# Performance work log

Hardware: AMD Instinct MI355X
Metric: run time of the kernel (lower is better)

## Reference

```python
import jax, jax.numpy as jnp
import numpy as np

N_NODES = 6144
IN_FEATURES = 256
N_HEADS = 4
N_HIDDEN = 64  # out_features, concat=False
LEAKY_SLOPE = 0.2
NEG_INF = -9e16


def setup_inputs() -> dict:
    key = jax.random.key(0)
    k1, k2, k3, k4 = jax.random.split(key, 4)
    h = jax.random.normal(k1, (N_NODES, IN_FEATURES), dtype=jnp.float32)
    adj_mat = jax.random.randint(k2, (N_NODES, N_NODES), 0, 2, dtype=jnp.int32)
    W = jax.random.normal(k3, (IN_FEATURES, N_HEADS * N_HIDDEN), dtype=jnp.float32) * 0.06
    a = jax.random.normal(k4, (N_HEADS, 2 * N_HIDDEN, 1), dtype=jnp.float32) * 0.1
    return {"h": h, "adj_mat": adj_mat, "W": W, "a": a}


def reference(h, adj_mat, W, a):
    n_nodes = h.shape[0]
    # linear transform, dropout is identity in eval mode
    ht = (h @ W).reshape(n_nodes, N_HEADS, N_HIDDEN).transpose(1, 0, 2)  # [H, N, d]
    a_src = a[:, :N_HIDDEN, 0]   # [H, d]
    a_tgt = a[:, N_HIDDEN:, 0]   # [H, d]
    src = jnp.einsum('hnd,hd->hn', ht, a_src)  # [H, N]
    tgt = jnp.einsum('hnd,hd->hn', ht, a_tgt)  # [H, N]
    e = src[:, :, None] + tgt[:, None, :]       # [H, N, N]
    e = jnp.where(e >= 0, e, LEAKY_SLOPE * e)    # leaky relu
    e = jnp.where(adj_mat[None, :, :] > 0, e, jnp.float32(NEG_INF))
    attention = jax.nn.softmax(e, axis=-1)       # [H, N, N]
    h_prime = jnp.einsum('hij,hjd->hid', attention, ht)  # [H, N, d]
    return h_prime.mean(axis=0)                  # [N, d] (concat=False)
```

## Files before the change

kernel.cpp:

```cpp
#include <hip/hip_runtime.h>
#include <hip/hip_bf16.h>

#define N_NODES 6144
#define IN_F 256
#define N_HEADS 4
#define N_HID 64
#define JS 8
#define JLEN (N_NODES / JS)
#define NW (JLEN / 32)
#define SM_STRIDE 28

typedef __attribute__((ext_vector_type(4))) float floatx4;
typedef _Float16 half2_t __attribute__((ext_vector_type(2)));
typedef _Float16 half8_t __attribute__((ext_vector_type(8)));
typedef __attribute__((ext_vector_type(4))) unsigned uint4_t;
typedef short short2v __attribute__((ext_vector_type(2)));

__global__ __launch_bounds__(256) void ht_gemm_kernel(
    const float* __restrict__ h, const float* __restrict__ W,
    const float* __restrict__ a, short* __restrict__ htF,
    float* __restrict__ srcv, unsigned* __restrict__ tE1pk, unsigned* __restrict__ tE2pk)
{
    __shared__ float As[32][34];
    __shared__ float Bs[32][68];
    __shared__ float redS[32][16];
    __shared__ float redT[32][16];
    __shared__ unsigned short eh1[32], eh2[32];

    const int head = blockIdx.y;
    const int i0 = blockIdx.x * 32;
    const int tid = threadIdx.x;
    const int tx = tid & 15, ty = tid >> 4;

    float acc[2][4] = {};

    for (int k0 = 0; k0 < IN_F; k0 += 32) {
        __syncthreads();
        {
            const int m = tid >> 3, kq = tid & 7;
            const float4 v = *(const float4*)(h + (i0 + m) * IN_F + k0 + kq * 4);
            As[kq*4+0][m] = v.x; As[kq*4+1][m] = v.y;
            As[kq*4+2][m] = v.z; As[kq*4+3][m] = v.w;
        }
        #pragma unroll
        for (int it = 0; it < 2; ++it) {
            int l = it * 256 + tid;
            int k = l >> 4, nq = l & 15;
            *(float4*)&Bs[k][nq*4] = *(const float4*)(W + (k0 + k) * 256 + head * 64 + nq * 4);
        }
        __syncthreads();
        #pragma unroll
        for (int kk = 0; kk < 32; ++kk) {
            const float2 av = *(const float2*)&As[kk][ty*2];
            const float4 bv = *(const float4*)&Bs[kk][tx*4];
            const float aa[2] = {av.x, av.y};
            const float bb[4] = {bv.x, bv.y, bv.z, bv.w};
            #pragma unroll
            for (int r = 0; r < 2; ++r)
                #pragma unroll
                for (int c = 0; c < 4; ++c)
                    acc[r][c] = fmaf(aa[r], bb[c], acc[r][c]);
        }
    }

    #pragma unroll
    for (int r = 0; r < 2; ++r)
        #pragma unroll
        for (int c2 = 0; c2 < 4; ++c2) {
            const int d = tx * 4 + c2;
            const int j = i0 + ty * 2 + r;
            const int jt = j >> 5, q = (j >> 3) & 3, u = j & 7;
            const int c = d >> 4, n = d & 15;
            const size_t F = (((((size_t)head * 192 + jt) * 4 + c) * 16 + n) * 4 + q) * 8 + u;
            const _Float16 hv = (_Float16)acc[r][c2];
            htF[F] = *(const short*)&hv;
        }

    float as_[4], at_[4];
    #pragma unroll
    for (int c = 0; c < 4; ++c) {
        as_[c] = a[head * 128 + tx * 4 + c];
        at_[c] = a[head * 128 + 64 + tx * 4 + c];
    }
    #pragma unroll
    for (int r = 0; r < 2; ++r) {
        float ps = 0.f, pt = 0.f;
        #pragma unroll
        for (int c = 0; c < 4; ++c) {
            ps = fmaf(acc[r][c], as_[c], ps);
            pt = fmaf(acc[r][c], at_[c], pt);
        }
        redS[ty*2+r][tx] = ps;
        redT[ty*2+r][tx] = pt;
    }
    __syncthreads();
    if (tid < 64) {
        const int row = tid & 31;
        const float* src = (tid < 32) ? &redS[row][0] : &redT[row][0];
        float s = 0.f;
        #pragma unroll
        for (int x = 0; x < 16; ++x) s += src[x];
        if (tid < 32) {
            srcv[head * N_NODES + i0 + row] = s;
        } else {
            const _Float16 E1 = (_Float16)__expf(s);
            const _Float16 E2 = (_Float16)__expf(0.2f * s);
            eh1[row] = *(const unsigned short*)&E1;
            eh2[row] = *(const unsigned short*)&E2;
        }
    }
    __syncthreads();
    if (tid < 16) {
        const unsigned v1 = (unsigned)eh1[2*tid] | ((unsigned)eh1[2*tid+1] << 16);
        const unsigned v2 = (unsigned)eh2[2*tid] | ((unsigned)eh2[2*tid+1] << 16);
        tE1pk[head * (N_NODES/2) + i0/2 + tid] = v1;
        tE2pk[head * (N_NODES/2) + i0/2 + tid] = v2;
    }
}

__global__ __launch_bounds__(256, 3) void gat_main_kernel(
    const int* __restrict__ adj, const short* __restrict__ htF,
    const float* __restrict__ srcv, const unsigned* __restrict__ tE1pk,
    const unsigned* __restrict__ tE2pk,
    float* __restrict__ pnum, float* __restrict__ pden)
{
    __shared__ unsigned smask[64 * SM_STRIDE];
    __shared__ unsigned sE1[4 * 384], sE2[4 * 384];

    const int bid = blockIdx.x;
    const int xcd = bid & 7;
    const int idx = bid >> 3;
    const int jc = idx / 12;
    const int rb0 = ((idx % 12) * 8 + xcd) * 64;

    const int lane = threadIdx.x;
    const int head = threadIdx.y;
    const int m = lane & 15, quad = lane >> 4;
    const int jbase = jc * JLEN;
    const int tid = head * 64 + lane;

    const int* adjb = adj + (size_t)rb0 * N_NODES + jbase + lane;
    for (int k0 = 0; k0 < 192; k0 += 8) {
        int v[8];
        #pragma unroll
        for (int s = 0; s < 8; ++s) {
            const int f = (k0 + s) * 4 + head;
            const int r = f / 12, W = f % 12;
            v[s] = adjb[(size_t)r * N_NODES + W * 64];
        }
        #pragma unroll
        for (int s = 0; s < 8; ++s) {
            const unsigned long long b = __ballot(v[s] > 0);
            const int f = (k0 + s) * 4 + head;
            const int r = f / 12, W = f % 12;
            if (lane == 0)
                *(unsigned long long*)&smask[r * SM_STRIDE + 2 * W] = b;
        }
    }
    #pragma unroll
    for (int it = 0; it < 3; ++it) {
        const int flat = it * 256 + tid;
        const int isE2 = flat >= 384;
        const int f = isE2 ? flat - 384 : flat;
        const int hh = f / 96, w4 = f % 96;
        const unsigned* g = (isE2 ? tE2pk : tE1pk) + hh * (N_NODES/2) + (jbase >> 1) + w4 * 4;
        const uint4_t v = *(const uint4_t*)g;
        unsigned* dst = (isE2 ? sE2 : sE1) + hh * 384 + w4 * 4;
        dst[0] = v.x; dst[1] = v.y; dst[2] = v.z; dst[3] = v.w;
    }
    __syncthreads();

    half2_t e1s[4], e2s[4];
    #pragma unroll
    for (int t = 0; t < 4; ++t) {
        const float sv = srcv[head * N_NODES + rb0 + t * 16 + m];
        const _Float16 a1 = (_Float16)__expf(sv);
        const _Float16 a2 = (_Float16)__expf(0.2f * sv);
        e1s[t] = (half2_t){a1, a1};
        e2s[t] = (half2_t){a2, a2};
    }

    const short* fb = htF + ((size_t)(head * 192 + (jbase >> 5)) * 4) * 512 + (m * 4 + quad) * 8;
    const unsigned* mrow = &smask[m * SM_STRIDE];
    const unsigned* pe1 = &sE1[head * 384];
    const unsigned* pe2 = &sE2[head * 384];

    half8_t bones;
    #pragma unroll
    for (int u = 0; u < 8; ++u) bones[u] = (_Float16)1.0f;

    floatx4 accN[4][4];
    floatx4 accD[4];
    #pragma unroll
    for (int t = 0; t < 4; ++t) {
        accD[t] = (floatx4){0,0,0,0};
        #pragma unroll
        for (int c = 0; c < 4; ++c) accN[t][c] = (floatx4){0,0,0,0};
    }

    half8_t bn[4];
    #pragma unroll
    for (int c = 0; c < 4; ++c) bn[c] = *(const half8_t*)(fb + c * 512);

    for (int w = 0; w < NW; ++w) {
        half8_t bc[4];
        #pragma unroll
        for (int c = 0; c < 4; ++c) bc[c] = bn[c];
        const int wn = (w + 1 < NW) ? (w + 1) : w;
        #pragma unroll
        for (int c = 0; c < 4; ++c)
            bn[c] = *(const half8_t*)(fb + (size_t)wn * 2048 + c * 512);

        const uint4_t E1 = *(const uint4_t*)(pe1 + w * 16 + quad * 4);
        const uint4_t E2 = *(const uint4_t*)(pe2 + w * 16 + quad * 4);
        const unsigned E1a[4] = {E1.x, E1.y, E1.z, E1.w};
        const unsigned E2a[4] = {E2.x, E2.y, E2.z, E2.w};

        #pragma unroll
        for (int t = 0; t < 4; ++t) {
            const unsigned bits = (mrow[t * (16*SM_STRIDE) + w] >> (quad * 8)) & 0xffu;
            const short2v tt = __builtin_bit_cast(short2v, bits * 0x10001u);
            uint4_t af_u;
            #pragma unroll
            for (int p = 0; p < 4; ++p) {
                const short2v shl = (p == 0) ? (short2v){15,14} : (p == 1) ? (short2v){13,12}
                                 : (p == 2) ? (short2v){11,10} : (short2v){9,8};
                const short2v k = (tt << shl) >> (short2v){15,15};
                const half2_t p1 = __builtin_bit_cast(half2_t, E1a[p]) * e1s[t];
                const half2_t p2 = __builtin_bit_cast(half2_t, E2a[p]) * e2s[t];
                const half2_t mx = __builtin_elementwise_max(p1, p2);
                const unsigned r = __builtin_bit_cast(unsigned, mx) & __builtin_bit_cast(unsigned, k);
                if (p == 0) af_u.x = r; else if (p == 1) af_u.y = r;
                else if (p == 2) af_u.z = r; else af_u.w = r;
            }
            const half8_t af = __builtin_bit_cast(half8_t, af_u);
            #pragma unroll
            for (int c = 0; c < 4; ++c)
                accN[t][c] = __builtin_amdgcn_mfma_f32_16x16x32_f16(af, bc[c], accN[t][c], 0, 0, 0);
            accD[t] = __builtin_amdgcn_mfma_f32_16x16x32_f16(af, bones, accD[t], 0, 0, 0);
        }
    }

    const int slot = jc * N_HEADS + head;
    #pragma unroll
    for (int t = 0; t < 4; ++t) {
        if (m == 0) {
            #pragma unroll
            for (int r = 0; r < 4; ++r)
                pden[slot * N_NODES + rb0 + t * 16 + quad * 4 + r] = accD[t][r];
        }
        #pragma unroll
        for (int r = 0; r < 4; ++r) {
            const int gi = rb0 + t * 16 + quad * 4 + r;
            float* np_ = pnum + ((size_t)slot * N_NODES + gi) * N_HID + m;
            np_[0]  = accN[t][0][r];
            np_[16] = accN[t][1][r];
            np_[32] = accN[t][2][r];
            np_[48] = accN[t][3][r];
        }
    }
}

__global__ __launch_bounds__(256) void finalize_kernel(
    const float* __restrict__ pnum, const float* __restrict__ pden,
    float* __restrict__ out)
{
    const int idx = blockIdx.x * 256 + threadIdx.x;
    if (idx >= N_NODES * 16) return;
    const int i = idx >> 4;
    const int d4 = (idx & 15) * 4;
    float sx = 0.f, sy = 0.f, sz = 0.f, sw = 0.f;
    #pragma unroll
    for (int hh = 0; hh < N_HEADS; ++hh) {
        float nx = 0.f, ny = 0.f, nz = 0.f, nw_ = 0.f, ds = 0.f;
        #pragma unroll
        for (int jc = 0; jc < JS; ++jc) {
            const int slot = jc * N_HEADS + hh;
            const float4 v = *(const float4*)(pnum + ((size_t)slot * N_NODES + i) * N_HID + d4);
            nx += v.x; ny += v.y; nz += v.z; nw_ += v.w;
            ds += pden[slot * N_NODES + i];
        }
        const float r = 1.0f / ds;
        sx += nx * r; sy += ny * r; sz += nz * r; sw += nw_ * r;
    }
    float4 o; o.x = 0.25f * sx; o.y = 0.25f * sy; o.z = 0.25f * sz; o.w = 0.25f * sw;
    *(float4*)(out + (size_t)i * N_HID + d4) = o;
}

extern "C" void kernel_launch(void* const* d_in, const int* in_sizes, int n_in,
                              void* d_out, int out_size, void* d_ws, size_t ws_size,
                              hipStream_t stream)
{
    const float* h   = (const float*)d_in[0];
    const int*   adj = (const int*)d_in[1];
    const float* W   = (const float*)d_in[2];
    const float* a   = (const float*)d_in[3];
    float* out = (float*)d_out;

    char* ws = (char*)d_ws;
    short* htF = (short*)ws;
    size_t off = (size_t)N_HEADS * N_HID * N_NODES * 2;
    float* srcv = (float*)(ws + off);        off += (size_t)N_HEADS * N_NODES * 4;
    unsigned* tE1pk = (unsigned*)(ws + off); off += (size_t)N_HEADS * (N_NODES/2) * 4;
    unsigned* tE2pk = (unsigned*)(ws + off); off += (size_t)N_HEADS * (N_NODES/2) * 4;
    float* pnum = (float*)(ws + off);        off += (size_t)JS * N_HEADS * N_NODES * N_HID * 4;
    float* pden = (float*)(ws + off);

    ht_gemm_kernel<<<dim3(N_NODES / 32, N_HEADS), 256, 0, stream>>>(h, W, a, htF, srcv, tE1pk, tE2pk);
    gat_main_kernel<<<768, dim3(64, 4), 0, stream>>>(
        adj, htF, srcv, tE1pk, tE2pk, pnum, pden);
    finalize_kernel<<<dim3((N_NODES * 16 + 255) / 256), 256, 0, stream>>>(pnum, pden, out);
}
```

Before: 270.7 us.

## Pack adjacency mask in prep kernel and reduce split-K partials with atomics

Moves adjacency-to-bitmask packing out of the attention kernel into extra blocks of the GEMM prep kernel, which also zero the accumulators. The main kernel now uses 32-row tiles with higher occupancy, loads the precomputed mask, and prefetches E1/E2 directly from global memory. Split-K partial numerators and denominators are combined with float atomic adds instead of separate per-slice buffers, shrinking the finalize pass. This trades large partial-buffer traffic for atomic contention and nondeterministic summation order.

```diff
diff --git a/kernel.cpp b/kernel.cpp
--- a/kernel.cpp
+++ b/kernel.cpp
@@ -8,7 +8,10 @@
 #define JS 8
 #define JLEN (N_NODES / JS)
 #define NW (JLEN / 32)
-#define SM_STRIDE 28
+#define SM_STRIDE 25
+#define PACK_BLOCKS 768
+#define ACC_F32 (N_HEADS * N_NODES * N_HID + N_HEADS * N_NODES)
+#define ZERO_F4_PER_BLOCK 520
 
 typedef __attribute__((ext_vector_type(4))) float floatx4;
 typedef _Float16 half2_t __attribute__((ext_vector_type(2)));
@@ -16,10 +19,16 @@
 typedef __attribute__((ext_vector_type(4))) unsigned uint4_t;
 typedef short short2v __attribute__((ext_vector_type(2)));
 
-__global__ __launch_bounds__(256) void ht_gemm_kernel(
+__device__ __forceinline__ void atomAddF32(float* p, float v) {
+    unsafeAtomicAdd(p, v);
+}
+
+__global__ __launch_bounds__(256) void prep_kernel(
     const float* __restrict__ h, const float* __restrict__ W,
-    const float* __restrict__ a, short* __restrict__ htF,
-    float* __restrict__ srcv, unsigned* __restrict__ tE1pk, unsigned* __restrict__ tE2pk)
+    const float* __restrict__ a, const int* __restrict__ adj,
+    short* __restrict__ htF, float* __restrict__ srcv,
+    unsigned* __restrict__ tE1pk, unsigned* __restrict__ tE2pk,
+    unsigned long long* __restrict__ gmask, float* __restrict__ accZero)
 {
     __shared__ float As[32][34];
     __shared__ float Bs[32][68];
@@ -27,8 +36,39 @@
     __shared__ float redT[32][16];
     __shared__ unsigned short eh1[32], eh2[32];
 
-    const int head = blockIdx.y;
-    const int i0 = blockIdx.x * 32;
+    if (blockIdx.x < PACK_BLOCKS) {
+        {
+            float4* z = (float4*)accZero + (size_t)blockIdx.x * ZERO_F4_PER_BLOCK;
+            const float4 zv = {0.f, 0.f, 0.f, 0.f};
+            for (int i = threadIdx.x; i < ZERO_F4_PER_BLOCK; i += 256) z[i] = zv;
+        }
+        const int lane = threadIdx.x & 63;
+        const int wave = threadIdx.x >> 6;
+        const int wbase = (blockIdx.x * 4 + wave) * 192;
+        for (int k0 = 0; k0 < 192; k0 += 16) {
+            int v[16];
+            #pragma unroll
+            for (int s = 0; s < 16; ++s) {
+                const int widx = wbase + k0 + s;
+                const int r = widx / 96, c = widx % 96;
+                v[s] = adj[(size_t)r * N_NODES + c * 64 + lane];
+            }
+            #pragma unroll
+            for (int s = 0; s < 16; ++s) {
+                const unsigned long long b = __ballot(v[s] > 0);
+                const int widx = wbase + k0 + s;
+                const int r = widx / 96, c = widx % 96;
+                const int jcp = c / 12, wl = c % 12;
+                if (lane == 0)
+                    gmask[((size_t)jcp * N_NODES + r) * 12 + wl] = b;
+            }
+        }
+        return;
+    }
+
+    const int gbx = blockIdx.x - PACK_BLOCKS;
+    const int head = gbx & 3;
+    const int i0 = (gbx >> 2) * 32;
     const int tid = threadIdx.x;
     const int tx = tid & 15, ty = tid >> 4;
 
@@ -118,20 +158,19 @@
     }
 }
 
-__global__ __launch_bounds__(256, 3) void gat_main_kernel(
-    const int* __restrict__ adj, const short* __restrict__ htF,
+__global__ __launch_bounds__(256, 4) void gat_main_kernel(
+    const unsigned* __restrict__ gmask32, const short* __restrict__ htF,
     const float* __restrict__ srcv, const unsigned* __restrict__ tE1pk,
     const unsigned* __restrict__ tE2pk,
-    float* __restrict__ pnum, float* __restrict__ pden)
+    float* __restrict__ accNg, float* __restrict__ accDg)
 {
-    __shared__ unsigned smask[64 * SM_STRIDE];
-    __shared__ unsigned sE1[4 * 384], sE2[4 * 384];
+    __shared__ unsigned smask[32 * SM_STRIDE];
 
     const int bid = blockIdx.x;
     const int xcd = bid & 7;
     const int idx = bid >> 3;
-    const int jc = idx / 12;
-    const int rb0 = ((idx % 12) * 8 + xcd) * 64;
+    const int jc = idx / 24;
+    const int rb0 = ((idx % 24) * 8 + xcd) * 32;
 
     const int lane = threadIdx.x;
     const int head = threadIdx.y;
@@ -139,40 +178,19 @@
     const int jbase = jc * JLEN;
     const int tid = head * 64 + lane;
 
-    const int* adjb = adj + (size_t)rb0 * N_NODES + jbase + lane;
-    for (int k0 = 0; k0 < 192; k0 += 8) {
-        int v[8];
-        #pragma unroll
-        for (int s = 0; s < 8; ++s) {
-            const int f = (k0 + s) * 4 + head;
-            const int r = f / 12, W = f % 12;
-            v[s] = adjb[(size_t)r * N_NODES + W * 64];
-        }
-        #pragma unroll
-        for (int s = 0; s < 8; ++s) {
-            const unsigned long long b = __ballot(v[s] > 0);
-            const int f = (k0 + s) * 4 + head;
-            const int r = f / 12, W = f % 12;
-            if (lane == 0)
-                *(unsigned long long*)&smask[r * SM_STRIDE + 2 * W] = b;
-        }
-    }
-    #pragma unroll
-    for (int it = 0; it < 3; ++it) {
-        const int flat = it * 256 + tid;
-        const int isE2 = flat >= 384;
-        const int f = isE2 ? flat - 384 : flat;
-        const int hh = f / 96, w4 = f % 96;
-        const unsigned* g = (isE2 ? tE2pk : tE1pk) + hh * (N_NODES/2) + (jbase >> 1) + w4 * 4;
-        const uint4_t v = *(const uint4_t*)g;
-        unsigned* dst = (isE2 ? sE2 : sE1) + hh * 384 + w4 * 4;
-        dst[0] = v.x; dst[1] = v.y; dst[2] = v.z; dst[3] = v.w;
+    {
+        const unsigned* g = gmask32 + ((size_t)jc * N_NODES + rb0) * 24;
+        #pragma unroll
+        for (int it = 0; it < 3; ++it) {
+            const int f = it * 256 + tid;
+            smask[(f / 24) * SM_STRIDE + (f % 24)] = g[f];
+        }
     }
     __syncthreads();
 
-    half2_t e1s[4], e2s[4];
-    #pragma unroll
-    for (int t = 0; t < 4; ++t) {
+    half2_t e1s[2], e2s[2];
+    #pragma unroll
+    for (int t = 0; t < 2; ++t) {
         const float sv = srcv[head * N_NODES + rb0 + t * 16 + m];
         const _Float16 a1 = (_Float16)__expf(sv);
         const _Float16 a2 = (_Float16)__expf(0.2f * sv);
@@ -181,18 +199,17 @@
     }
 
     const short* fb = htF + ((size_t)(head * 192 + (jbase >> 5)) * 4) * 512 + (m * 4 + quad) * 8;
-    const unsigned* mrow = &smask[m * SM_STRIDE];
-    const unsigned* pe1 = &sE1[head * 384];
-    const unsigned* pe2 = &sE2[head * 384];
+    const unsigned* pe1 = tE1pk + head * (N_NODES/2) + (jbase >> 1) + quad * 4;
+    const unsigned* pe2 = tE2pk + head * (N_NODES/2) + (jbase >> 1) + quad * 4;
 
     half8_t bones;
     #pragma unroll
     for (int u = 0; u < 8; ++u) bones[u] = (_Float16)1.0f;
 
-    floatx4 accN[4][4];
-    floatx4 accD[4];
-    #pragma unroll
-    for (int t = 0; t < 4; ++t) {
+    floatx4 accN[2][4];
+    floatx4 accD[2];
+    #pragma unroll
+    for (int t = 0; t < 2; ++t) {
         accD[t] = (floatx4){0,0,0,0};
         #pragma unroll
         for (int c = 0; c < 4; ++c) accN[t][c] = (floatx4){0,0,0,0};
@@ -201,24 +218,28 @@
     half8_t bn[4];
     #pragma unroll
     for (int c = 0; c < 4; ++c) bn[c] = *(const half8_t*)(fb + c * 512);
+    uint4_t E1n = *(const uint4_t*)pe1;
+    uint4_t E2n = *(const uint4_t*)pe2;
 
     for (int w = 0; w < NW; ++w) {
         half8_t bc[4];
         #pragma unroll
         for (int c = 0; c < 4; ++c) bc[c] = bn[c];
+        const uint4_t E1 = E1n, E2 = E2n;
+
         const int wn = (w + 1 < NW) ? (w + 1) : w;
         #pragma unroll
         for (int c = 0; c < 4; ++c)
             bn[c] = *(const half8_t*)(fb + (size_t)wn * 2048 + c * 512);
-
-        const uint4_t E1 = *(const uint4_t*)(pe1 + w * 16 + quad * 4);
-        const uint4_t E2 = *(const uint4_t*)(pe2 + w * 16 + quad * 4);
+        E1n = *(const uint4_t*)(pe1 + wn * 16);
+        E2n = *(const uint4_t*)(pe2 + wn * 16);
+
         const unsigned E1a[4] = {E1.x, E1.y, E1.z, E1.w};
         const unsigned E2a[4] = {E2.x, E2.y, E2.z, E2.w};
 
         #pragma unroll
-        for (int t = 0; t < 4; ++t) {
-            const unsigned bits = (mrow[t * (16*SM_STRIDE) + w] >> (quad * 8)) & 0xffu;
+        for (int t = 0; t < 2; ++t) {
+            const unsigned bits = (smask[(t * 16 + m) * SM_STRIDE + w] >> (quad * 8)) & 0xffu;
             const short2v tt = __builtin_bit_cast(short2v, bits * 0x10001u);
             uint4_t af_u;
             #pragma unroll
@@ -241,28 +262,24 @@
         }
     }
 
-    const int slot = jc * N_HEADS + head;
-    #pragma unroll
-    for (int t = 0; t < 4; ++t) {
-        if (m == 0) {
-            #pragma unroll
-            for (int r = 0; r < 4; ++r)
-                pden[slot * N_NODES + rb0 + t * 16 + quad * 4 + r] = accD[t][r];
-        }
+    const size_t nb = (size_t)head * N_NODES;
+    #pragma unroll
+    for (int t = 0; t < 2; ++t) {
         #pragma unroll
         for (int r = 0; r < 4; ++r) {
             const int gi = rb0 + t * 16 + quad * 4 + r;
-            float* np_ = pnum + ((size_t)slot * N_NODES + gi) * N_HID + m;
-            np_[0]  = accN[t][0][r];
-            np_[16] = accN[t][1][r];
-            np_[32] = accN[t][2][r];
-            np_[48] = accN[t][3][r];
+            if (m == 0) atomAddF32(&accDg[nb + gi], accD[t][r]);
+            float* np_ = accNg + (nb + gi) * N_HID + m;
+            atomAddF32(np_ + 0,  accN[t][0][r]);
+            atomAddF32(np_ + 16, accN[t][1][r]);
+            atomAddF32(np_ + 32, accN[t][2][r]);
+            atomAddF32(np_ + 48, accN[t][3][r]);
         }
     }
 }
 
 __global__ __launch_bounds__(256) void finalize_kernel(
-    const float* __restrict__ pnum, const float* __restrict__ pden,
+    const float* __restrict__ accNg, const float* __restrict__ accDg,
     float* __restrict__ out)
 {
     const int idx = blockIdx.x * 256 + threadIdx.x;
@@ -272,16 +289,9 @@
     float sx = 0.f, sy = 0.f, sz = 0.f, sw = 0.f;
     #pragma unroll
     for (int hh = 0; hh < N_HEADS; ++hh) {
-        float nx = 0.f, ny = 0.f, nz = 0.f, nw_ = 0.f, ds = 0.f;
-        #pragma unroll
-        for (int jc = 0; jc < JS; ++jc) {
-            const int slot = jc * N_HEADS + hh;
-            const float4 v = *(const float4*)(pnum + ((size_t)slot * N_NODES + i) * N_HID + d4);
-            nx += v.x; ny += v.y; nz += v.z; nw_ += v.w;
-            ds += pden[slot * N_NODES + i];
-        }
-        const float r = 1.0f / ds;
-        sx += nx * r; sy += ny * r; sz += nz * r; sw += nw_ * r;
+        const float4 v = *(const float4*)(accNg + ((size_t)hh * N_NODES + i) * N_HID + d4);
+        const float r = 1.0f / accDg[hh * N_NODES + i];
+        sx += v.x * r; sy += v.y * r; sz += v.z * r; sw += v.w * r;
     }
     float4 o; o.x = 0.25f * sx; o.y = 0.25f * sy; o.z = 0.25f * sz; o.w = 0.25f * sw;
     *(float4*)(out + (size_t)i * N_HID + d4) = o;
@@ -303,11 +313,14 @@
     float* srcv = (float*)(ws + off);        off += (size_t)N_HEADS * N_NODES * 4;
     unsigned* tE1pk = (unsigned*)(ws + off); off += (size_t)N_HEADS * (N_NODES/2) * 4;
     unsigned* tE2pk = (unsigned*)(ws + off); off += (size_t)N_HEADS * (N_NODES/2) * 4;
-    float* pnum = (float*)(ws + off);        off += (size_t)JS * N_HEADS * N_NODES * N_HID * 4;
-    float* pden = (float*)(ws + off);
-
-    ht_gemm_kernel<<<dim3(N_NODES / 32, N_HEADS), 256, 0, stream>>>(h, W, a, htF, srcv, tE1pk, tE2pk);
-    gat_main_kernel<<<768, dim3(64, 4), 0, stream>>>(
-        adj, htF, srcv, tE1pk, tE2pk, pnum, pden);
-    finalize_kernel<<<dim3((N_NODES * 16 + 255) / 256), 256, 0, stream>>>(pnum, pden, out);
-}
+    unsigned long long* gmask = (unsigned long long*)(ws + off);
+    off += (size_t)JS * N_NODES * 12 * 8;
+    float* accN = (float*)(ws + off);        off += (size_t)N_HEADS * N_NODES * N_HID * 4;
+    float* accD = (float*)(ws + off);        off += (size_t)N_HEADS * N_NODES * 4;
+
+    prep_kernel<<<PACK_BLOCKS + (N_NODES / 32) * N_HEADS, 256, 0, stream>>>(
+        h, W, a, adj, htF, srcv, tE1pk, tE2pk, gmask, accN );
+    gat_main_kernel<<<1536, dim3(64, 4), 0, stream>>>(
+        (const unsigned*)gmask, htF, srcv, tE1pk, tE2pk, accN, accD);
+    finalize_kernel<<<(N_NODES * 16 + 255) / 256, 256, 0, stream>>>(accN, accD, out);
+}
```

Result: slower. 304.2 us (+12.4%).

## Split main kernel row tiles across 8 waves and shrink finalize blocks

Applied to the files above, without the earlier changes.

Doubles the main GAT kernel's block to 8 waves, so each head gets two waves that each own half of the 64-row tile. This halves per-wave accumulator registers and gives more waves to hide latency while the mask and E-table loads are shared across more threads. Each wave now loads the same htF B-fragments as its partner, which doubles those global/L2 reads. The finalize kernel also moves to 128-thread blocks.

```diff
diff --git a/kernel.cpp b/kernel.cpp
--- a/kernel.cpp
+++ b/kernel.cpp
@@ -118,7 +118,7 @@
     }
 }
 
-__global__ __launch_bounds__(256, 3) void gat_main_kernel(
+__global__ __launch_bounds__(512, 6) void gat_main_kernel(
     const int* __restrict__ adj, const short* __restrict__ htF,
     const float* __restrict__ srcv, const unsigned* __restrict__ tE1pk,
     const unsigned* __restrict__ tE2pk,
@@ -134,50 +134,55 @@
     const int rb0 = ((idx % 12) * 8 + xcd) * 64;
 
     const int lane = threadIdx.x;
-    const int head = threadIdx.y;
+    const int wy = threadIdx.y;
+    const int head = wy & 3;
+    const int half = wy >> 2;
     const int m = lane & 15, quad = lane >> 4;
     const int jbase = jc * JLEN;
-    const int tid = head * 64 + lane;
+    const int tid = wy * 64 + lane;
 
     const int* adjb = adj + (size_t)rb0 * N_NODES + jbase + lane;
-    for (int k0 = 0; k0 < 192; k0 += 8) {
+    for (int k0 = 0; k0 < 96; k0 += 8) {
         int v[8];
         #pragma unroll
         for (int s = 0; s < 8; ++s) {
-            const int f = (k0 + s) * 4 + head;
+            const int f = (k0 + s) * 8 + wy;
             const int r = f / 12, W = f % 12;
             v[s] = adjb[(size_t)r * N_NODES + W * 64];
         }
         #pragma unroll
         for (int s = 0; s < 8; ++s) {
             const unsigned long long b = __ballot(v[s] > 0);
-            const int f = (k0 + s) * 4 + head;
+            const int f = (k0 + s) * 8 + wy;
             const int r = f / 12, W = f % 12;
             if (lane == 0)
                 *(unsigned long long*)&smask[r * SM_STRIDE + 2 * W] = b;
         }
     }
     #pragma unroll
-    for (int it = 0; it < 3; ++it) {
-        const int flat = it * 256 + tid;
-        const int isE2 = flat >= 384;
-        const int f = isE2 ? flat - 384 : flat;
-        const int hh = f / 96, w4 = f % 96;
-        const unsigned* g = (isE2 ? tE2pk : tE1pk) + hh * (N_NODES/2) + (jbase >> 1) + w4 * 4;
-        const uint4_t v = *(const uint4_t*)g;
-        unsigned* dst = (isE2 ? sE2 : sE1) + hh * 384 + w4 * 4;
-        dst[0] = v.x; dst[1] = v.y; dst[2] = v.z; dst[3] = v.w;
+    for (int it = 0; it < 2; ++it) {
+        const int flat = it * 512 + tid;
+        if (flat < 768) {
+            const int isE2 = flat >= 384;
+            const int f = isE2 ? flat - 384 : flat;
+            const int hh = f / 96, w4 = f % 96;
+            const unsigned* g = (isE2 ? tE2pk : tE1pk) + hh * (N_NODES/2) + (jbase >> 1) + w4 * 4;
+            const uint4_t v = *(const uint4_t*)g;
+            unsigned* dst = (isE2 ? sE2 : sE1) + hh * 384 + w4 * 4;
+            *(uint4_t*)dst = v;
+        }
     }
     __syncthreads();
 
-    half2_t e1s[4], e2s[4];
-    #pragma unroll
-    for (int t = 0; t < 4; ++t) {
-        const float sv = srcv[head * N_NODES + rb0 + t * 16 + m];
+    half2_t e1s[2], e2s[2];
+    #pragma unroll
+    for (int tt = 0; tt < 2; ++tt) {
+        const int t2 = half * 2 + tt;
+        const float sv = srcv[head * N_NODES + rb0 + t2 * 16 + m];
         const _Float16 a1 = (_Float16)__expf(sv);
         const _Float16 a2 = (_Float16)__expf(0.2f * sv);
-        e1s[t] = (half2_t){a1, a1};
-        e2s[t] = (half2_t){a2, a2};
+        e1s[tt] = (half2_t){a1, a1};
+        e2s[tt] = (half2_t){a2, a2};
     }
 
     const short* fb = htF + ((size_t)(head * 192 + (jbase >> 5)) * 4) * 512 + (m * 4 + quad) * 8;
@@ -189,13 +194,13 @@
     #pragma unroll
     for (int u = 0; u < 8; ++u) bones[u] = (_Float16)1.0f;
 
-    floatx4 accN[4][4];
-    floatx4 accD[4];
-    #pragma unroll
-    for (int t = 0; t < 4; ++t) {
-        accD[t] = (floatx4){0,0,0,0};
-        #pragma unroll
-        for (int c = 0; c < 4; ++c) accN[t][c] = (floatx4){0,0,0,0};
+    floatx4 accN[2][4];
+    floatx4 accD[2];
+    #pragma unroll
+    for (int tt = 0; tt < 2; ++tt) {
+        accD[tt] = (floatx4){0,0,0,0};
+        #pragma unroll
+        for (int c = 0; c < 4; ++c) accN[tt][c] = (floatx4){0,0,0,0};
     }
 
     half8_t bn[4];
@@ -217,17 +222,18 @@
         const unsigned E2a[4] = {E2.x, E2.y, E2.z, E2.w};
 
         #pragma unroll
-        for (int t = 0; t < 4; ++t) {
-            const unsigned bits = (mrow[t * (16*SM_STRIDE) + w] >> (quad * 8)) & 0xffu;
-            const short2v tt = __builtin_bit_cast(short2v, bits * 0x10001u);
+        for (int tt = 0; tt < 2; ++tt) {
+            const int t2 = half * 2 + tt;
+            const unsigned bits = (mrow[t2 * (16*SM_STRIDE) + w] >> (quad * 8)) & 0xffu;
+            const short2v tv = __builtin_bit_cast(short2v, bits * 0x10001u);
             uint4_t af_u;
             #pragma unroll
             for (int p = 0; p < 4; ++p) {
                 const short2v shl = (p == 0) ? (short2v){15,14} : (p == 1) ? (short2v){13,12}
                                  : (p == 2) ? (short2v){11,10} : (short2v){9,8};
-                const short2v k = (tt << shl) >> (short2v){15,15};
-                const half2_t p1 = __builtin_bit_cast(half2_t, E1a[p]) * e1s[t];
-                const half2_t p2 = __builtin_bit_cast(half2_t, E2a[p]) * e2s[t];
+                const short2v k = (tv << shl) >> (short2v){15,15};
+                const half2_t p1 = __builtin_bit_cast(half2_t, E1a[p]) * e1s[tt];
+                const half2_t p2 = __builtin_bit_cast(half2_t, E2a[p]) * e2s[tt];
                 const half2_t mx = __builtin_elementwise_max(p1, p2);
                 const unsigned r = __builtin_bit_cast(unsigned, mx) & __builtin_bit_cast(unsigned, k);
                 if (p == 0) af_u.x = r; else if (p == 1) af_u.y = r;
@@ -236,36 +242,37 @@
             const half8_t af = __builtin_bit_cast(half8_t, af_u);
             #pragma unroll
             for (int c = 0; c < 4; ++c)
-                accN[t][c] = __builtin_amdgcn_mfma_f32_16x16x32_f16(af, bc[c], accN[t][c], 0, 0, 0);
-            accD[t] = __builtin_amdgcn_mfma_f32_16x16x32_f16(af, bones, accD[t], 0, 0, 0);
+                accN[tt][c] = __builtin_amdgcn_mfma_f32_16x16x32_f16(af, bc[c], accN[tt][c], 0, 0, 0);
+            accD[tt] = __builtin_amdgcn_mfma_f32_16x16x32_f16(af, bones, accD[tt], 0, 0, 0);
         }
     }
 
     const int slot = jc * N_HEADS + head;
     #pragma unroll
-    for (int t = 0; t < 4; ++t) {
+    for (int tt = 0; tt < 2; ++tt) {
+        const int t2 = half * 2 + tt;
         if (m == 0) {
             #pragma unroll
             for (int r = 0; r < 4; ++r)
-                pden[slot * N_NODES + rb0 + t * 16 + quad * 4 + r] = accD[t][r];
+                pden[slot * N_NODES + rb0 + t2 * 16 + quad * 4 + r] = accD[tt][r];
         }
         #pragma unroll
         for (int r = 0; r < 4; ++r) {
-            const int gi = rb0 + t * 16 + quad * 4 + r;
+            const int gi = rb0 + t2 * 16 + quad * 4 + r;
             float* np_ = pnum + ((size_t)slot * N_NODES + gi) * N_HID + m;
-            np_[0]  = accN[t][0][r];
-            np_[16] = accN[t][1][r];
-            np_[32] = accN[t][2][r];
-            np_[48] = accN[t][3][r];
+            np_[0]  = accN[tt][0][r];
+            np_[16] = accN[tt][1][r];
+            np_[32] = accN[tt][2][r];
+            np_[48] = accN[tt][3][r];
         }
     }
 }
 
-__global__ __launch_bounds__(256) void finalize_kernel(
+__global__ __launch_bounds__(128) void finalize_kernel(
     const float* __restrict__ pnum, const float* __restrict__ pden,
     float* __restrict__ out)
 {
-    const int idx = blockIdx.x * 256 + threadIdx.x;
+    const int idx = blockIdx.x * 128 + threadIdx.x;
     if (idx >= N_NODES * 16) return;
     const int i = idx >> 4;
     const int d4 = (idx & 15) * 4;
@@ -307,7 +314,7 @@
     float* pden = (float*)(ws + off);
 
     ht_gemm_kernel<<<dim3(N_NODES / 32, N_HEADS), 256, 0, stream>>>(h, W, a, htF, srcv, tE1pk, tE2pk);
-    gat_main_kernel<<<768, dim3(64, 4), 0, stream>>>(
+    gat_main_kernel<<<768, dim3(64, 8), 0, stream>>>(
         adj, htF, srcv, tE1pk, tE2pk, pnum, pden);
-    finalize_kernel<<<dim3((N_NODES * 16 + 255) / 256), 256, 0, stream>>>(pnum, pden, out);
+    finalize_kernel<<<(N_NODES * 16 + 127) / 128, 128, 0, stream>>>(pnum, pden, out);
 }
```

Measured after the change: 424.8 us. 57.0% more time.
